# Kernel optimization log

Hardware: AMD Instinct MI355X
Metric: run time of the kernel (lower is better)

## Reference

```python
import jax, jax.numpy as jnp
import numpy as np
from jax import lax

DIM = 192
HEADS = 8
HID = int(DIM * 4.0)

def setup_inputs() -> dict:
    key = jax.random.key(0)
    ks = jax.random.split(key, 10)
    b, c, h, w = 4, DIM, 256, DIM  # w must equal dim for the Mlp over last axis
    x = jax.random.normal(ks[0], (b, c, h, w), dtype=jnp.float32)
    return {
        "x": x,
        "ln1_w": jnp.ones((DIM,), jnp.float32),
        "ln1_b": jnp.zeros((DIM,), jnp.float32),
        "temperature": jnp.ones((HEADS, 1, 1), jnp.float32),
        "qkv_w": jax.random.normal(ks[1], (3 * DIM, DIM), jnp.float32) * 0.02,
        "dw_w": jax.random.normal(ks[2], (3 * DIM, 1, 3, 3), jnp.float32) * 0.1,
        "proj_w": jax.random.normal(ks[3], (DIM, DIM), jnp.float32) * 0.02,
        "ln2_w": jnp.ones((DIM,), jnp.float32),
        "ln2_b": jnp.zeros((DIM,), jnp.float32),
        "fc1_w": jax.random.normal(ks[4], (HID, DIM), jnp.float32) * 0.02,
        "fc1_b": jnp.zeros((HID,), jnp.float32),
        "fc2_w": jax.random.normal(ks[5], (DIM, HID), jnp.float32) * 0.02,
        "fc2_b": jnp.zeros((DIM,), jnp.float32),
    }

def _layernorm_chan(x, w, b):
    # WithBias LayerNorm over the channel axis, per spatial location (to_3d -> LN -> to_4d)
    mu = jnp.mean(x, axis=1, keepdims=True)
    var = jnp.mean((x - mu) ** 2, axis=1, keepdims=True)
    y = (x - mu) / jnp.sqrt(var + 1e-5)
    return y * w[None, :, None, None] + b[None, :, None, None]

def _l2norm(x, axis=-1, eps=1e-12):
    n = jnp.sqrt(jnp.sum(x * x, axis=axis, keepdims=True))
    return x / jnp.maximum(n, eps)

def _attention(x, temperature, qkv_w, dw_w, proj_w):
    b, c, h, w = x.shape
    # 1x1 conv (pointwise GEMM) then 3x3 depthwise conv
    qkv = jnp.einsum('oc,bchw->bohw', qkv_w, x)
    qkv = lax.conv_general_dilated(qkv, dw_w, window_strides=(1, 1), padding='SAME',
                                   feature_group_count=3 * c,
                                   dimension_numbers=('NCHW', 'OIHW', 'NCHW'))
    q, k, v = jnp.split(qkv, 3, axis=1)
    ch = c // HEADS
    q = q.reshape(b, HEADS, ch, h * w)
    k = k.reshape(b, HEADS, ch, h * w)
    v = v.reshape(b, HEADS, ch, h * w)
    q = _l2norm(q)
    k = _l2norm(k)
    attn = jnp.einsum('bhcn,bhdn->bhcd', q, k) * temperature  # [b,H,ch,ch] channel attention
    attn = jax.nn.softmax(attn, axis=-1)
    out = jnp.einsum('bhcd,bhdn->bhcn', attn, v).reshape(b, c, h, w)
    return jnp.einsum('oc,bchw->bohw', proj_w, out)

def _mlp(x, fc1_w, fc1_b, fc2_w, fc2_b):
    # nn.Linear applied on the LAST axis (w == dim), matching the original quirk
    h1 = jnp.einsum('bchw,ow->bcho', x, fc1_w) + fc1_b
    h1 = jax.nn.gelu(h1, approximate=False)
    return jnp.einsum('bcho,do->bchd', h1, fc2_w) + fc2_b

def reference(x, ln1_w, ln1_b, temperature, qkv_w, dw_w, proj_w, ln2_w, ln2_b, fc1_w, fc1_b, fc2_w, fc2_b):
    x = x + _attention(_layernorm_chan(x, ln1_w, ln1_b), temperature, qkv_w, dw_w, proj_w)
    x = x + _mlp(_layernorm_chan(x, ln2_w, ln2_b), fc1_w, fc1_b, fc2_w, fc2_b)
    return x
```

## Files before the change

### kernel.cpp

```cpp
#include <hip/hip_runtime.h>
#include <math.h>

#define SSP   49152
#define HDIM  256
#define WDIM  192
#define CDIM  192
#define NHEAD 8
#define CH    24
#define OC3   576
#define HIDF  768
#define NB    4
#define SCCH  24

typedef short bf16x8 __attribute__((ext_vector_type(8)));
typedef short bf16x4 __attribute__((ext_vector_type(4)));
typedef float f32x4  __attribute__((ext_vector_type(4)));

__device__ inline short f2bf(float f) {
  unsigned u = __float_as_uint(f);
  u += 0x7fffu + ((u >> 16) & 1u);
  return (short)(u >> 16);
}
__device__ inline float bf2f(short h) {
  return __uint_as_float(((unsigned)(unsigned short)h) << 16);
}

__global__ __launch_bounds__(256) void cvt_bf16(const float* __restrict__ in,
                                                short* __restrict__ out, int n) {
  int i = blockIdx.x * 256 + threadIdx.x;
  if (i < n) out[i] = f2bf(in[i]);
}

template <bool TRANS>
__global__ __launch_bounds__(256) void ln_bf16(const float* __restrict__ x,
                                               const float* __restrict__ w,
                                               const float* __restrict__ bia,
                                               short* __restrict__ outp) {
  __shared__ float xs[192][68];
  __shared__ float ps[4][64], pq[4][64], mus[64], rst[64];
  const int tid = threadIdx.x;
  const int s0 = blockIdx.x * 64;
  const float* xb = x + (size_t)blockIdx.y * CDIM * SSP;
  short* outb = outp + (size_t)blockIdx.y * CDIM * SSP;
#pragma unroll
  for (int it = 0; it < 12; ++it) {
    int u = it * 256 + tid;
    int c = u >> 4, q = u & 15;
    float4 v = *(const float4*)(xb + (size_t)c * SSP + s0 + q * 4);
    *(float4*)&xs[c][q * 4] = v;
  }
  __syncthreads();
  {
    int s = tid & 63, p = tid >> 6;
    float sm = 0.f, sq = 0.f;
    for (int c = p * 48; c < p * 48 + 48; ++c) {
      float v = xs[c][s]; sm += v; sq += v * v;
    }
    ps[p][s] = sm; pq[p][s] = sq;
  }
  __syncthreads();
  if (tid < 64) {
    float sm = ps[0][tid] + ps[1][tid] + ps[2][tid] + ps[3][tid];
    float sq = pq[0][tid] + pq[1][tid] + pq[2][tid] + pq[3][tid];
    float mu = sm * (1.f / CDIM);
    mus[tid] = mu;
    rst[tid] = rsqrtf(sq * (1.f / CDIM) - mu * mu + 1e-5f);
  }
  __syncthreads();
  if (TRANS) {
#pragma unroll
    for (int it = 0; it < 6; ++it) {
      int u = it * 256 + tid;
      int c8 = u >> 6, sr = u & 63;
      float mu = mus[sr], r = rst[sr];
      bf16x8 o;
#pragma unroll
      for (int j = 0; j < 8; ++j) {
        int c = c8 * 8 + j;
        o[j] = f2bf((xs[c][sr] - mu) * r * w[c] + bia[c]);
      }
      *(bf16x8*)(outb + (size_t)(s0 + sr) * CDIM + c8 * 8) = o;
    }
  } else {
#pragma unroll
    for (int it = 0; it < 6; ++it) {
      int u = it * 256 + tid;
      int c = u >> 3, sv = u & 7;
      float wc = w[c], bc = bia[c];
      bf16x8 o;
#pragma unroll
      for (int j = 0; j < 8; ++j) {
        int s = sv * 8 + j;
        o[j] = f2bf((xs[c][s] - mus[s]) * rst[s] * wc + bc);
      }
      *(bf16x8*)(outb + (size_t)c * SSP + s0 + sv * 8) = o;
    }
  }
}

template <int BM, int BN, int WM, int WN, bool RESID, bool OUT_BF16>
__global__ __launch_bounds__(256) void mfma_gemm(
    const short* __restrict__ A, const short* __restrict__ B,
    const float* __restrict__ resid, void* __restrict__ Cv,
    int M, int N, int K, long long strideB, long long strideC) {
  constexpr int BK = 32, PAD = 40;
  constexpr int WTM = BM / WM, WTN = BN / WN;
  constexpr int FM = WTM / 16, FN = WTN / 16;
  static_assert(WM * WN == 4 && BM % 64 == 0 && BN % 64 == 0, "cfg");
  __shared__ short As[BM * PAD];
  __shared__ short Bs[BN * PAD];
  const int tid = threadIdx.x;
  const int m0 = blockIdx.y * BM, n0 = blockIdx.x * BN;
  const long long z = blockIdx.z;
  const short* Bz = B + z * strideB;
  const int w = tid >> 6, lane = tid & 63;
  const int wm = w / WN, wn = w % WN;
  const int r16 = lane & 15, kg = lane >> 4;
  const int arow = tid >> 2, akc = tid & 3;

  f32x4 acc[FM][FN] = {};

  for (int k0 = 0; k0 < K; k0 += BK) {
#pragma unroll
    for (int i = 0; i < BM; i += 64) {
      bf16x8 v = *(const bf16x8*)(A + (size_t)(m0 + i + arow) * K + k0 + akc * 8);
      *(bf16x8*)(&As[(i + arow) * PAD + akc * 8]) = v;
    }
#pragma unroll
    for (int i = 0; i < BN; i += 64) {
      bf16x8 v = *(const bf16x8*)(Bz + (size_t)(n0 + i + arow) * K + k0 + akc * 8);
      *(bf16x8*)(&Bs[(i + arow) * PAD + akc * 8]) = v;
    }
    __syncthreads();
    bf16x8 af[FM], bfr[FN];
#pragma unroll
    for (int i = 0; i < FM; ++i)
      af[i] = *(bf16x8*)(&As[(wm * WTM + i * 16 + r16) * PAD + kg * 8]);
#pragma unroll
    for (int j = 0; j < FN; ++j)
      bfr[j] = *(bf16x8*)(&Bs[(wn * WTN + j * 16 + r16) * PAD + kg * 8]);
#pragma unroll
    for (int i = 0; i < FM; ++i)
#pragma unroll
      for (int j = 0; j < FN; ++j)
        acc[i][j] = __builtin_amdgcn_mfma_f32_16x16x32_bf16(af[i], bfr[j], acc[i][j], 0, 0, 0);
    __syncthreads();
  }

  float* Cf = (float*)Cv + z * strideC;
  short* Ch = (short*)Cv + z * strideC;
  const float* R = RESID ? resid + z * strideC : nullptr;
#pragma unroll
  for (int i = 0; i < FM; ++i) {
#pragma unroll
    for (int j = 0; j < FN; ++j) {
#pragma unroll
      for (int t = 0; t < 4; ++t) {
        int m = m0 + wm * WTM + i * 16 + kg * 4 + t;
        int n = n0 + wn * WTN + j * 16 + r16;
        float v = acc[i][j][t];
        size_t idx = (size_t)m * N + n;
        if (RESID) v += R[idx];
        if (OUT_BF16) Ch[idx] = f2bf(v); else Cf[idx] = v;
      }
    }
  }
}

__global__ __launch_bounds__(256) void dwconv_tile(const short* __restrict__ in,
                                                   const float* __restrict__ w9,
                                                   short* __restrict__ out) {
  __shared__ short tile[34][208];
  const int tid = threadIdx.x;
  const int ch = blockIdx.x >> 3;
  const int slab = blockIdx.x & 7;
  const int o = ch % OC3;
  const int y0 = slab * 32;
  float wr[9];
#pragma unroll
  for (int i = 0; i < 9; ++i) wr[i] = w9[o * 9 + i];
  const short* ip = in + (size_t)ch * SSP;

  if (tid < 34) { tile[tid][7] = 0; tile[tid][200] = 0; }
#pragma unroll
  for (int i = 0; i < 4; ++i) {
    int idx = i * 256 + tid;
    if (idx < 816) {
      int row = idx / 24, cx = idx - row * 24;
      int gy = y0 + row - 1;
      bf16x8 v = {};
      if (gy >= 0 && gy < HDIM) v = *(const bf16x8*)(ip + gy * WDIM + cx * 8);
      *(bf16x8*)(&tile[row][8 + cx * 8]) = v;
    }
  }
  __syncthreads();

  short* op = out + (size_t)ch * SSP;
#pragma unroll
  for (int g = 0; g < 3; ++g) {
    int G = g * 256 + tid;
    int r = G / 24, cx = G - (G / 24) * 24;
    int cb = cx * 8 + 7;
    float a[10], b[10], c[10];
#pragma unroll
    for (int d = 0; d < 10; ++d) {
      a[d] = bf2f(tile[r][cb + d]);
      b[d] = bf2f(tile[r + 1][cb + d]);
      c[d] = bf2f(tile[r + 2][cb + d]);
    }
    bf16x8 ov;
#pragma unroll
    for (int j = 0; j < 8; ++j) {
      float acc = wr[0] * a[j] + wr[1] * a[j + 1] + wr[2] * a[j + 2]
                + wr[3] * b[j] + wr[4] * b[j + 1] + wr[5] * b[j + 2]
                + wr[6] * c[j] + wr[7] * c[j + 1] + wr[8] * c[j + 2];
      ov[j] = f2bf(acc);
    }
    *(bf16x8*)(op + (y0 + r) * WDIM + cx * 8) = ov;
  }
}

__global__ __launch_bounds__(256) void scores_stage1(const short* __restrict__ D,
                                                     float* __restrict__ pdot,
                                                     float* __restrict__ qss,
                                                     float* __restrict__ kss) {
  int ch = blockIdx.x, h = blockIdx.y, b = blockIdx.z;
  __shared__ float qs[24][260];
  __shared__ float ks[24][260];
  int tid = threadIdx.x;
  int w = tid >> 6, lane = tid & 63;
  int c0 = w * 6;
  float acc[6] = {0.f, 0.f, 0.f, 0.f, 0.f, 0.f};
  float ssacc = 0.f;
  const short* qb = D + ((size_t)b * OC3 + h * CH) * SSP;
  const short* kb = D + ((size_t)b * OC3 + CDIM + h * CH) * SSP;
  for (int it = 0; it < 8; ++it) {
    int s0 = ch * 2048 + it * 256;
#pragma unroll
    for (int p = 0; p < 3; ++p) {
      int u = p * 256 + tid;
      int row = u >> 5, col8 = u & 31;
      bf16x8 qv = *(const bf16x8*)(qb + (size_t)row * SSP + s0 + col8 * 8);
      bf16x8 kv = *(const bf16x8*)(kb + (size_t)row * SSP + s0 + col8 * 8);
#pragma unroll
      for (int j = 0; j < 8; ++j) {
        qs[row][col8 * 8 + j] = bf2f(qv[j]);
        ks[row][col8 * 8 + j] = bf2f(kv[j]);
      }
    }
    __syncthreads();
    if (w < 2 && lane < 24) {
      const float (*src)[260] = (w == 0) ? qs : ks;
      for (int s = 0; s < 256; s += 4) {
        float4 v = *(const float4*)&src[lane][s];
        ssacc += v.x * v.x + v.y * v.y + v.z * v.z + v.w * v.w;
      }
    }
    if (lane < 24) {
      for (int s = 0; s < 256; s += 4) {
        float4 kv = *(float4*)&ks[lane][s];
#pragma unroll
        for (int i = 0; i < 6; ++i) {
          float4 qv = *(float4*)&qs[c0 + i][s];
          acc[i] += qv.x * kv.x + qv.y * kv.y + qv.z * kv.z + qv.w * kv.w;
        }
      }
    }
    __syncthreads();
  }
  if (lane < 24) {
    float* pb = pdot + (size_t)b * (NHEAD * CH * CH * SCCH);
#pragma unroll
    for (int i = 0; i < 6; ++i)
      pb[(((size_t)h * CH + (c0 + i)) * CH + lane) * SCCH + ch] = acc[i];
    if (w == 0) qss[(((size_t)b * NHEAD + h) * CH + lane) * SCCH + ch] = ssacc;
    if (w == 1) kss[(((size_t)b * NHEAD + h) * CH + lane) * SCCH + ch] = ssacc;
  }
}

__global__ void scores_reduce(const float* __restrict__ pdot,
                              const float* __restrict__ qss,
                              const float* __restrict__ kss,
                              const float* __restrict__ temp,
                              float* __restrict__ atn) {
  int c = blockIdx.x, h = blockIdx.y, b = blockIdx.z;
  int tid = threadIdx.x;
  __shared__ float row[24];
  if (tid < 24) {
    const float* p = pdot + (size_t)b * (NHEAD * CH * CH * SCCH) +
                     (((size_t)h * CH + c) * CH + tid) * SCCH;
    float s = 0.f;
#pragma unroll
    for (int i = 0; i < SCCH; ++i) s += p[i];
    const float* pq = qss + (((size_t)b * NHEAD + h) * CH + c) * SCCH;
    const float* pk = kss + (((size_t)b * NHEAD + h) * CH + tid) * SCCH;
    float sq = 0.f, sk = 0.f;
#pragma unroll
    for (int i = 0; i < SCCH; ++i) { sq += pq[i]; sk += pk[i]; }
    float rq = 1.f / fmaxf(sqrtf(sq), 1e-12f);
    float rk = 1.f / fmaxf(sqrtf(sk), 1e-12f);
    row[tid] = s * rq * rk * temp[h];
  }
  __syncthreads();
  if (tid < 24) {
    float mx = -1e30f;
    for (int d = 0; d < 24; ++d) mx = fmaxf(mx, row[d]);
    float sum = 0.f;
    for (int d = 0; d < 24; ++d) sum += expf(row[d] - mx);
    atn[((size_t)b * NHEAD + h) * 576 + c * CH + tid] = expf(row[tid] - mx) / sum;
  }
}

__global__ __launch_bounds__(256) void attn_pv_bf16(const short* __restrict__ D,
                                                    const float* __restrict__ atn,
                                                    short* __restrict__ pvt) {
  int nb = blockIdx.x, h = blockIdx.y, b = blockIdx.z;
  __shared__ float aL[24][24];
  int tid = threadIdx.x;
  const float* ab = atn + ((size_t)b * NHEAD + h) * 576;
  for (int i = tid; i < 576; i += 256) aL[i / 24][i % 24] = ab[i];
  __syncthreads();
  int n = nb * 256 + tid;
  const short* vb = D + ((size_t)b * OC3 + 2 * CDIM + h * CH) * SSP + n;
  float vv[24];
#pragma unroll
  for (int d = 0; d < 24; ++d) vv[d] = bf2f(vb[(size_t)d * SSP]);
  short* ob = pvt + (size_t)b * SSP * CDIM + (size_t)n * CDIM + h * CH;
  bf16x8 o0, o1, o2;
#pragma unroll
  for (int cc = 0; cc < 24; ++cc) {
    float s = 0.f;
#pragma unroll
    for (int d = 0; d < 24; ++d) s += aL[cc][d] * vv[d];
    short bv = f2bf(s);
    if (cc < 8) o0[cc & 7] = bv; else if (cc < 16) o1[cc & 7] = bv; else o2[cc & 7] = bv;
  }
  *(bf16x8*)(ob) = o0;
  *(bf16x8*)(ob + 8) = o1;
  *(bf16x8*)(ob + 16) = o2;
}

__global__ __launch_bounds__(256) void mlp_fused(const short* __restrict__ y2,
                                                 const short* __restrict__ w1,
                                                 const short* __restrict__ w2,
                                                 const float* __restrict__ b1,
                                                 const float* __restrict__ b2,
                                                 float* __restrict__ out) {
  __shared__ short w1s[64 * 200];
  __shared__ short w2s[192 * 72];
  __shared__ short h1s[64 * 72];
  const int tid = threadIdx.x;
  const int m0 = blockIdx.x * 64;
  const int w = tid >> 6, lane = tid & 63;
  const int r16 = lane & 15, kg = lane >> 4;
  const int wm = w >> 1, wn = w & 1;

  int s1r[6], s1c[6], s2r[6], s2c[6];
#pragma unroll
  for (int it = 0; it < 6; ++it) {
    int u = it * 256 + tid;
    s1r[it] = u / 24; s1c[it] = u % 24;
    s2r[it] = u / 8;  s2c[it] = u % 8;
  }

  bf16x8 afr[2][6];
#pragma unroll
  for (int ks = 0; ks < 6; ++ks)
#pragma unroll
    for (int i = 0; i < 2; ++i)
      afr[i][ks] = *(const bf16x8*)(y2 + (size_t)(m0 + wm * 32 + i * 16 + r16) * CDIM + ks * 32 + kg * 8);

#pragma unroll
  for (int it = 0; it < 6; ++it) {
    *(bf16x8*)(&w1s[s1r[it] * 200 + s1c[it] * 8]) =
        *(const bf16x8*)(w1 + (size_t)s1r[it] * CDIM + s1c[it] * 8);
    *(bf16x8*)(&w2s[s2r[it] * 72 + s2c[it] * 8]) =
        *(const bf16x8*)(w2 + (size_t)s2r[it] * HIDF + s2c[it] * 8);
  }
  __syncthreads();

  f32x4 bacc[2][6] = {};
  bf16x8 rw1[6], rw2[6];

  for (int hc = 0; hc < 12; ++hc) {
    if (hc < 11) {
#pragma unroll
      for (int it = 0; it < 6; ++it) {
        rw1[it] = *(const bf16x8*)(w1 + (size_t)((hc + 1) * 64 + s1r[it]) * CDIM + s1c[it] * 8);
        rw2[it] = *(const bf16x8*)(w2 + (size_t)s2r[it] * HIDF + (hc + 1) * 64 + s2c[it] * 8);
      }
    }
    f32x4 pacc[2][2] = {};
#pragma unroll
    for (int ks = 0; ks < 6; ++ks) {
      bf16x8 bg[2];
#pragma unroll
      for (int j = 0; j < 2; ++j)
        bg[j] = *(bf16x8*)(&w1s[(wn * 32 + j * 16 + r16) * 200 + ks * 32 + kg * 8]);
#pragma unroll
      for (int i = 0; i < 2; ++i)
#pragma unroll
        for (int j = 0; j < 2; ++j)
          pacc[i][j] = __builtin_amdgcn_mfma_f32_16x16x32_bf16(bg[j], afr[i][ks], pacc[i][j], 0, 0, 0);
    }
#pragma unroll
    for (int i = 0; i < 2; ++i) {
      int mr = wm * 32 + i * 16 + r16;
#pragma unroll
      for (int j = 0; j < 2; ++j) {
        int hid0 = wn * 32 + j * 16 + kg * 4;
        bf16x4 pk;
#pragma unroll
        for (int t = 0; t < 4; ++t) {
          float v = pacc[i][j][t] + b1[hc * 64 + hid0 + t];
          v = 0.5f * v * (1.f + erff(v * 0.70710678118654752f));
          pk[t] = f2bf(v);
        }
        *(bf16x4*)(&h1s[mr * 72 + hid0]) = pk;
      }
    }
    __syncthreads();
    if (hc < 11) {
#pragma unroll
      for (int it = 0; it < 6; ++it)
        *(bf16x8*)(&w1s[s1r[it] * 200 + s1c[it] * 8]) = rw1[it];
    }
#pragma unroll
    for (int ks = 0; ks < 2; ++ks) {
      bf16x8 a2[2];
#pragma unroll
      for (int i = 0; i < 2; ++i)
        a2[i] = *(bf16x8*)(&h1s[(wm * 32 + i * 16 + r16) * 72 + ks * 32 + kg * 8]);
#pragma unroll
      for (int j = 0; j < 6; ++j) {
        bf16x8 b2g = *(bf16x8*)(&w2s[(wn * 96 + j * 16 + r16) * 72 + ks * 32 + kg * 8]);
#pragma unroll
        for (int i = 0; i < 2; ++i)
          bacc[i][j] = __builtin_amdgcn_mfma_f32_16x16x32_bf16(a2[i], b2g, bacc[i][j], 0, 0, 0);
      }
    }
    __syncthreads();
    if (hc < 11) {
#pragma unroll
      for (int it = 0; it < 6; ++it)
        *(bf16x8*)(&w2s[s2r[it] * 72 + s2c[it] * 8]) = rw2[it];
    }
  }

#pragma unroll
  for (int i = 0; i < 2; ++i)
#pragma unroll
    for (int j = 0; j < 6; ++j)
#pragma unroll
      for (int t = 0; t < 4; ++t) {
        int m = m0 + wm * 32 + i * 16 + kg * 4 + t;
        int n = wn * 96 + j * 16 + r16;
        size_t idx = (size_t)m * CDIM + n;
        out[idx] = bacc[i][j][t] + b2[n] + out[idx];
      }
}

extern "C" void kernel_launch(void* const* d_in, const int* in_sizes, int n_in,
                              void* d_out, int out_size, void* d_ws, size_t ws_size,
                              hipStream_t stream) {
  const float* x      = (const float*)d_in[0];
  const float* ln1_w  = (const float*)d_in[1];
  const float* ln1_b  = (const float*)d_in[2];
  const float* temp   = (const float*)d_in[3];
  const float* qkv_w  = (const float*)d_in[4];
  const float* dw_w   = (const float*)d_in[5];
  const float* proj_w = (const float*)d_in[6];
  const float* ln2_w  = (const float*)d_in[7];
  const float* ln2_b  = (const float*)d_in[8];
  const float* fc1_w  = (const float*)d_in[9];
  const float* fc1_b  = (const float*)d_in[10];
  const float* fc2_w  = (const float*)d_in[11];
  const float* fc2_b  = (const float*)d_in[12];
  float* out = (float*)d_out;

  char* base = (char*)d_ws;
  short* wq  = (short*)base;
  short* wp  = wq + 110592;
  short* w1  = wp + 36864;
  short* w2  = w1 + 147456;
  float* pdot= (float*)(base + 890880);
  float* qss = (float*)(base + 2660352);
  float* kss = (float*)(base + 2734080);
  float* atn = (float*)(base + 2807808);
  short* Dv  = (short*)(base + 4194304);
  short* y1t = Dv;
  short* T   = (short*)(base + 230686720);
  short* pvt = T;
  short* y2  = (short*)(base + 457179136);

  cvt_bf16<<<dim3(432), 256, 0, stream>>>(qkv_w, wq, 110592);
  cvt_bf16<<<dim3(144), 256, 0, stream>>>(proj_w, wp, 36864);
  cvt_bf16<<<dim3(576), 256, 0, stream>>>(fc1_w, w1, 147456);
  cvt_bf16<<<dim3(576), 256, 0, stream>>>(fc2_w, w2, 147456);

  ln_bf16<true><<<dim3(SSP / 64, NB), 256, 0, stream>>>(x, ln1_w, ln1_b, y1t);
  mfma_gemm<64, 256, 1, 4, false, true><<<dim3(SSP / 256, OC3 / 64, NB), 256, 0, stream>>>(
      wq, y1t, nullptr, T, OC3, SSP, CDIM, (long long)SSP * CDIM, (long long)OC3 * SSP);
  dwconv_tile<<<dim3(NB * OC3 * 8), 256, 0, stream>>>(T, dw_w, Dv);
  scores_stage1<<<dim3(SCCH, NHEAD, NB), 256, 0, stream>>>(Dv, pdot, qss, kss);
  scores_reduce<<<dim3(CH, NHEAD, NB), 64, 0, stream>>>(pdot, qss, kss, temp, atn);
  attn_pv_bf16<<<dim3(SSP / 256, NHEAD, NB), 256, 0, stream>>>(Dv, atn, pvt);
  mfma_gemm<64, 256, 1, 4, true, false><<<dim3(SSP / 256, CDIM / 64, NB), 256, 0, stream>>>(
      wp, pvt, x, out, CDIM, SSP, CDIM, (long long)SSP * CDIM, (long long)CDIM * SSP);
  ln_bf16<false><<<dim3(SSP / 64, NB), 256, 0, stream>>>(out, ln2_w, ln2_b, y2);
  mlp_fused<<<dim3(196608 / 64), 256, 0, stream>>>(y2, w1, w2, fc1_b, fc2_b, out);
}
```

Baseline: 1.079 ms.

## Use direct global-to-LDS loads in GEMM and widen MLP blocks to 128 rows

The pointwise GEMM now stages A and B tiles with global_load_lds 16-byte transfers straight into unpadded LDS, so the loads no longer pass through registers. The fused MLP kernel doubles its row tile to 128 with 512 threads and keeps the y2 tile in LDS instead of registers. Each weight chunk loaded into LDS is now shared by twice as many rows. The costs are LDS bank conflicts from dropping the padding, higher LDS use that may lower occupancy, and an extra barrier per hidden chunk.

New measurement: 946.6 us. -12.3%, faster.

```diff
diff --git a/kernel.cpp b/kernel.cpp
--- a/kernel.cpp
+++ b/kernel.cpp
@@ -23,6 +23,12 @@
 }
 __device__ inline float bf2f(short h) {
   return __uint_as_float(((unsigned)(unsigned short)h) << 16);
+}
+
+__device__ inline void gl_lds16(const short* g, short* l) {
+  __builtin_amdgcn_global_load_lds(
+      (const __attribute__((address_space(1))) unsigned int*)g,
+      (__attribute__((address_space(3))) unsigned int*)l, 16, 0, 0);
 }
 
 __global__ __launch_bounds__(256) void cvt_bf16(const float* __restrict__ in,
@@ -98,51 +104,43 @@
   }
 }
 
-template <int BM, int BN, int WM, int WN, bool RESID, bool OUT_BF16>
+template <bool RESID, bool OUT_BF16>
 __global__ __launch_bounds__(256) void mfma_gemm(
     const short* __restrict__ A, const short* __restrict__ B,
     const float* __restrict__ resid, void* __restrict__ Cv,
     int M, int N, int K, long long strideB, long long strideC) {
-  constexpr int BK = 32, PAD = 40;
-  constexpr int WTM = BM / WM, WTN = BN / WN;
-  constexpr int FM = WTM / 16, FN = WTN / 16;
-  static_assert(WM * WN == 4 && BM % 64 == 0 && BN % 64 == 0, "cfg");
-  __shared__ short As[BM * PAD];
-  __shared__ short Bs[BN * PAD];
+  __shared__ short As[64 * 32];
+  __shared__ short Bs[256 * 32];
   const int tid = threadIdx.x;
-  const int m0 = blockIdx.y * BM, n0 = blockIdx.x * BN;
+  const int m0 = blockIdx.y * 64, n0 = blockIdx.x * 256;
   const long long z = blockIdx.z;
   const short* Bz = B + z * strideB;
   const int w = tid >> 6, lane = tid & 63;
-  const int wm = w / WN, wn = w % WN;
   const int r16 = lane & 15, kg = lane >> 4;
-  const int arow = tid >> 2, akc = tid & 3;
-
-  f32x4 acc[FM][FN] = {};
-
-  for (int k0 = 0; k0 < K; k0 += BK) {
-#pragma unroll
-    for (int i = 0; i < BM; i += 64) {
-      bf16x8 v = *(const bf16x8*)(A + (size_t)(m0 + i + arow) * K + k0 + akc * 8);
-      *(bf16x8*)(&As[(i + arow) * PAD + akc * 8]) = v;
-    }
-#pragma unroll
-    for (int i = 0; i < BN; i += 64) {
-      bf16x8 v = *(const bf16x8*)(Bz + (size_t)(n0 + i + arow) * K + k0 + akc * 8);
-      *(bf16x8*)(&Bs[(i + arow) * PAD + akc * 8]) = v;
+  const int arow = tid >> 2, ac4 = tid & 3;
+
+  f32x4 acc[4][4] = {};
+
+  for (int k0 = 0; k0 < K; k0 += 32) {
+    gl_lds16(A + (size_t)(m0 + arow) * K + k0 + ac4 * 8, As + w * 512);
+#pragma unroll
+    for (int p = 0; p < 4; ++p) {
+      int flat = p * 256 + tid;
+      int brow = flat >> 2, bc4 = flat & 3;
+      gl_lds16(Bz + (size_t)(n0 + brow) * K + k0 + bc4 * 8, Bs + p * 2048 + w * 512);
     }
     __syncthreads();
-    bf16x8 af[FM], bfr[FN];
-#pragma unroll
-    for (int i = 0; i < FM; ++i)
-      af[i] = *(bf16x8*)(&As[(wm * WTM + i * 16 + r16) * PAD + kg * 8]);
-#pragma unroll
-    for (int j = 0; j < FN; ++j)
-      bfr[j] = *(bf16x8*)(&Bs[(wn * WTN + j * 16 + r16) * PAD + kg * 8]);
-#pragma unroll
-    for (int i = 0; i < FM; ++i)
-#pragma unroll
-      for (int j = 0; j < FN; ++j)
+    bf16x8 af[4], bfr[4];
+#pragma unroll
+    for (int i = 0; i < 4; ++i)
+      af[i] = *(bf16x8*)(&As[(i * 16 + r16) * 32 + kg * 8]);
+#pragma unroll
+    for (int j = 0; j < 4; ++j)
+      bfr[j] = *(bf16x8*)(&Bs[(w * 64 + j * 16 + r16) * 32 + kg * 8]);
+#pragma unroll
+    for (int i = 0; i < 4; ++i)
+#pragma unroll
+      for (int j = 0; j < 4; ++j)
         acc[i][j] = __builtin_amdgcn_mfma_f32_16x16x32_bf16(af[i], bfr[j], acc[i][j], 0, 0, 0);
     __syncthreads();
   }
@@ -151,13 +149,13 @@
   short* Ch = (short*)Cv + z * strideC;
   const float* R = RESID ? resid + z * strideC : nullptr;
 #pragma unroll
-  for (int i = 0; i < FM; ++i) {
-#pragma unroll
-    for (int j = 0; j < FN; ++j) {
+  for (int i = 0; i < 4; ++i) {
+#pragma unroll
+    for (int j = 0; j < 4; ++j) {
 #pragma unroll
       for (int t = 0; t < 4; ++t) {
-        int m = m0 + wm * WTM + i * 16 + kg * 4 + t;
-        int n = n0 + wn * WTN + j * 16 + r16;
+        int m = m0 + i * 16 + kg * 4 + t;
+        int n = n0 + w * 64 + j * 16 + r16;
         float v = acc[i][j][t];
         size_t idx = (size_t)m * N + n;
         if (RESID) v += R[idx];
@@ -340,38 +338,37 @@
   *(bf16x8*)(ob + 16) = o2;
 }
 
-__global__ __launch_bounds__(256) void mlp_fused(const short* __restrict__ y2,
+__global__ __launch_bounds__(512) void mlp_fused(const short* __restrict__ y2,
                                                  const short* __restrict__ w1,
                                                  const short* __restrict__ w2,
                                                  const float* __restrict__ b1,
                                                  const float* __restrict__ b2,
                                                  float* __restrict__ out) {
+  __shared__ short y2s[128 * 200];
   __shared__ short w1s[64 * 200];
   __shared__ short w2s[192 * 72];
-  __shared__ short h1s[64 * 72];
+  __shared__ short h1s[128 * 72];
   const int tid = threadIdx.x;
-  const int m0 = blockIdx.x * 64;
+  const int m0 = blockIdx.x * 128;
   const int w = tid >> 6, lane = tid & 63;
   const int r16 = lane & 15, kg = lane >> 4;
   const int wm = w >> 1, wn = w & 1;
 
-  int s1r[6], s1c[6], s2r[6], s2c[6];
+  const int u0 = tid, u1 = 512 + tid, u2 = 1024 + tid;
+  const int s1r[3] = {u0 / 24, u1 / 24, u2 / 24};
+  const int s1c[3] = {u0 % 24, u1 % 24, u2 % 24};
+  const int s2r[3] = {u0 / 8, u1 / 8, u2 / 8};
+  const int s2c[3] = {u0 % 8, u1 % 8, u2 % 8};
+
 #pragma unroll
   for (int it = 0; it < 6; ++it) {
-    int u = it * 256 + tid;
-    s1r[it] = u / 24; s1c[it] = u % 24;
-    s2r[it] = u / 8;  s2c[it] = u % 8;
-  }
-
-  bf16x8 afr[2][6];
-#pragma unroll
-  for (int ks = 0; ks < 6; ++ks)
-#pragma unroll
-    for (int i = 0; i < 2; ++i)
-      afr[i][ks] = *(const bf16x8*)(y2 + (size_t)(m0 + wm * 32 + i * 16 + r16) * CDIM + ks * 32 + kg * 8);
-
-#pragma unroll
-  for (int it = 0; it < 6; ++it) {
+    int u = it * 512 + tid;
+    int row = u / 24, cx = u % 24;
+    *(bf16x8*)(&y2s[row * 200 + cx * 8]) =
+        *(const bf16x8*)(y2 + (size_t)(m0 + row) * CDIM + cx * 8);
+  }
+#pragma unroll
+  for (int it = 0; it < 3; ++it) {
     *(bf16x8*)(&w1s[s1r[it] * 200 + s1c[it] * 8]) =
         *(const bf16x8*)(w1 + (size_t)s1r[it] * CDIM + s1c[it] * 8);
     *(bf16x8*)(&w2s[s2r[it] * 72 + s2c[it] * 8]) =
@@ -380,12 +377,12 @@
   __syncthreads();
 
   f32x4 bacc[2][6] = {};
-  bf16x8 rw1[6], rw2[6];
+  bf16x8 rw1[3], rw2[3];
 
   for (int hc = 0; hc < 12; ++hc) {
     if (hc < 11) {
 #pragma unroll
-      for (int it = 0; it < 6; ++it) {
+      for (int it = 0; it < 3; ++it) {
         rw1[it] = *(const bf16x8*)(w1 + (size_t)((hc + 1) * 64 + s1r[it]) * CDIM + s1c[it] * 8);
         rw2[it] = *(const bf16x8*)(w2 + (size_t)s2r[it] * HIDF + (hc + 1) * 64 + s2c[it] * 8);
       }
@@ -393,7 +390,10 @@
     f32x4 pacc[2][2] = {};
 #pragma unroll
     for (int ks = 0; ks < 6; ++ks) {
-      bf16x8 bg[2];
+      bf16x8 af[2], bg[2];
+#pragma unroll
+      for (int i = 0; i < 2; ++i)
+        af[i] = *(bf16x8*)(&y2s[(wm * 32 + i * 16 + r16) * 200 + ks * 32 + kg * 8]);
 #pragma unroll
       for (int j = 0; j < 2; ++j)
         bg[j] = *(bf16x8*)(&w1s[(wn * 32 + j * 16 + r16) * 200 + ks * 32 + kg * 8]);
@@ -401,7 +401,7 @@
       for (int i = 0; i < 2; ++i)
 #pragma unroll
         for (int j = 0; j < 2; ++j)
-          pacc[i][j] = __builtin_amdgcn_mfma_f32_16x16x32_bf16(bg[j], afr[i][ks], pacc[i][j], 0, 0, 0);
+          pacc[i][j] = __builtin_amdgcn_mfma_f32_16x16x32_bf16(bg[j], af[i], pacc[i][j], 0, 0, 0);
     }
 #pragma unroll
     for (int i = 0; i < 2; ++i) {
@@ -420,11 +420,7 @@
       }
     }
     __syncthreads();
-    if (hc < 11) {
-#pragma unroll
-      for (int it = 0; it < 6; ++it)
-        *(bf16x8*)(&w1s[s1r[it] * 200 + s1c[it] * 8]) = rw1[it];
-    }
+
 #pragma unroll
     for (int ks = 0; ks < 2; ++ks) {
       bf16x8 a2[2];
@@ -440,10 +436,14 @@
       }
     }
     __syncthreads();
+
     if (hc < 11) {
 #pragma unroll
-      for (int it = 0; it < 6; ++it)
+      for (int it = 0; it < 3; ++it) {
+        *(bf16x8*)(&w1s[s1r[it] * 200 + s1c[it] * 8]) = rw1[it];
         *(bf16x8*)(&w2s[s2r[it] * 72 + s2c[it] * 8]) = rw2[it];
+      }
+      __syncthreads();
     }
   }
 
@@ -499,14 +499,14 @@
   cvt_bf16<<<dim3(576), 256, 0, stream>>>(fc2_w, w2, 147456);
 
   ln_bf16<true><<<dim3(SSP / 64, NB), 256, 0, stream>>>(x, ln1_w, ln1_b, y1t);
-  mfma_gemm<64, 256, 1, 4, false, true><<<dim3(SSP / 256, OC3 / 64, NB), 256, 0, stream>>>(
+  mfma_gemm<false, true><<<dim3(SSP / 256, OC3 / 64, NB), 256, 0, stream>>>(
       wq, y1t, nullptr, T, OC3, SSP, CDIM, (long long)SSP * CDIM, (long long)OC3 * SSP);
   dwconv_tile<<<dim3(NB * OC3 * 8), 256, 0, stream>>>(T, dw_w, Dv);
   scores_stage1<<<dim3(SCCH, NHEAD, NB), 256, 0, stream>>>(Dv, pdot, qss, kss);
   scores_reduce<<<dim3(CH, NHEAD, NB), 64, 0, stream>>>(pdot, qss, kss, temp, atn);
   attn_pv_bf16<<<dim3(SSP / 256, NHEAD, NB), 256, 0, stream>>>(Dv, atn, pvt);
-  mfma_gemm<64, 256, 1, 4, true, false><<<dim3(SSP / 256, CDIM / 64, NB), 256, 0, stream>>>(
+  mfma_gemm<true, false><<<dim3(SSP / 256, CDIM / 64, NB), 256, 0, stream>>>(
       wp, pvt, x, out, CDIM, SSP, CDIM, (long long)SSP * CDIM, (long long)CDIM * SSP);
   ln_bf16<false><<<dim3(SSP / 64, NB), 256, 0, stream>>>(out, ln2_w, ln2_b, y2);
-  mlp_fused<<<dim3(196608 / 64), 256, 0, stream>>>(y2, w1, w2, fc1_b, fc2_b, out);
-}
+  mlp_fused<<<dim3(196608 / 128), 512, 0, stream>>>(y2, w1, w2, fc1_b, fc2_b, out);
+}
```
